# Kernel tuning notes

Measured on AMD Instinct MI355X. Metric: run time of the kernel, lower is better.

The kernel has to match this reference:

```python
import jax, jax.numpy as jnp
import numpy as np

B, D, N_CLASSES = 8192, 128, 512
MARGIN, GAMMA = 0.25, 256.0
NEG_INF = -1e9  # effectively -inf; logits are O(gamma*2) ~ 512 in magnitude


def setup_inputs() -> dict:
    key = jax.random.key(0)
    k1, k2 = jax.random.split(key)
    feat = jax.random.normal(k1, (B, D), dtype=jnp.float32)
    label = jax.random.randint(k2, (B,), 0, N_CLASSES, dtype=jnp.int64)
    return {"feat": feat, "label": label}


def reference(feat, label):
    m, gamma = MARGIN, GAMMA
    O_p, O_n = 1.0 + m, -m
    delta_p, delta_n = 1.0 - m, m

    # L2-normalize rows (eps clamp as in F.normalize)
    norm = jnp.maximum(jnp.linalg.norm(feat, axis=1, keepdims=True), 1e-12)
    f = feat / norm
    sim = f @ f.T  # [B, B]

    same = label[:, None] == label[None, :]
    eye = jnp.eye(sim.shape[0], dtype=bool)
    pos_mask = same & ~eye
    neg_mask = ~same

    sim_d = jax.lax.stop_gradient(sim)  # .detach() in torch
    alpha_p = jax.nn.relu(O_p - sim_d)
    alpha_n = jax.nn.relu(sim_d - O_n)

    logit_p = -gamma * alpha_p * (sim - delta_p)
    logit_n = gamma * alpha_n * (sim - delta_n)

    # Per-row masked logsumexp over positives / negatives
    lse_p = jax.nn.logsumexp(jnp.where(pos_mask, logit_p, NEG_INF), axis=1)
    lse_n = jax.nn.logsumexp(jnp.where(neg_mask, logit_n, NEG_INF), axis=1)

    # Rows with no positives or no negatives are skipped in the original loop
    valid = pos_mask.any(axis=1) & neg_mask.any(axis=1)
    loss_i = jax.nn.softplus(lse_n + lse_p)
    n_valid = jnp.maximum(valid.sum(), 1)
    return jnp.sum(jnp.where(valid, loss_i, 0.0)) / n_valid
```

## Files before the change

### kernel.cpp

```cpp
#include <hip/hip_runtime.h>
#include <hip/hip_bf16.h>

typedef short bf16x8 __attribute__((ext_vector_type(8)));
typedef float f32x4 __attribute__((ext_vector_type(4)));

#define B_ROWS 8192
#define DIM 128
#define NCLS 512
#define MMAX 64
#define NSLICE 32
#define NEG_BLOCKS 1024

#define G2 369.32993f
#define LN2F 0.69314718056f

__global__ __launch_bounds__(256) void prep_k(const float* __restrict__ feat,
                                              const int* __restrict__ label,
                                              unsigned short* __restrict__ fb,
                                              float* __restrict__ fnorm,
                                              int* __restrict__ cls_cnt,
                                              int* __restrict__ member) {
    const int wv = threadIdx.x >> 6, ln = threadIdx.x & 63;
    const int row = blockIdx.x * 4 + wv;
    const float2* fr = (const float2*)(feat + row * DIM);
    float2 v = fr[ln];
    float ss = v.x * v.x + v.y * v.y;
    #pragma unroll
    for (int d = 1; d < 64; d <<= 1) ss += __shfl_xor(ss, d);
    const float inv = 1.0f / fmaxf(sqrtf(ss), 1e-12f);
    const float x = v.x * inv, y = v.y * inv;
    ((float2*)fnorm)[row * 64 + ln] = make_float2(x, y);
    __hip_bfloat16 hx = __float2bfloat16(x), hy = __float2bfloat16(y);
    unsigned int ux = *(unsigned short*)&hx, uy = *(unsigned short*)&hy;
    ((unsigned int*)fb)[row * 64 + ln] = ux | (uy << 16);

    if (blockIdx.x < 32) {
        const int idx = blockIdx.x * 256 + threadIdx.x;
        const int lbl = label[idx];
        const int p = atomicAdd(&cls_cnt[lbl], 1);
        if (p < MMAX) member[lbl * MMAX + p] = idx;
    }
}

__device__ __forceinline__ void epi4(f32x4 acc, float& M, float& S,
                                     bool diag, int lc, int lg) {
    float u0 = acc[0] + 0.25f; float w0 = fmaf(G2, acc[0], -0.25f * G2);
    float u1 = acc[1] + 0.25f; float w1 = fmaf(G2, acc[1], -0.25f * G2);
    float u2 = acc[2] + 0.25f; float w2 = fmaf(G2, acc[2], -0.25f * G2);
    float u3 = acc[3] + 0.25f; float w3 = fmaf(G2, acc[3], -0.25f * G2);
    float l0 = fmaxf(u0, 0.f) * w0, l1 = fmaxf(u1, 0.f) * w1;
    float l2 = fmaxf(u2, 0.f) * w2, l3 = fmaxf(u3, 0.f) * w3;
    if (diag) {
        const int base = lg * 4;
        l0 = (base + 0 == lc) ? -3.0e8f : l0;
        l1 = (base + 1 == lc) ? -3.0e8f : l1;
        l2 = (base + 2 == lc) ? -3.0e8f : l2;
        l3 = (base + 3 == lc) ? -3.0e8f : l3;
    }
    const float gm = fmaxf(fmaxf(l0, l1), fmaxf(l2, l3));
    if (__any(gm > M - 25.f)) {
        const float Mn = fmaxf(M, gm);
        const float r  = __builtin_amdgcn_exp2f(M - Mn);
        const float e0 = __builtin_amdgcn_exp2f(l0 - Mn);
        const float e1 = __builtin_amdgcn_exp2f(l1 - Mn);
        const float e2 = __builtin_amdgcn_exp2f(l2 - Mn);
        const float e3 = __builtin_amdgcn_exp2f(l3 - Mn);
        S = fmaf(S, r, e0) + e1 + e2 + e3;
        M = Mn;
    }
}

__global__ __launch_bounds__(256) void main_k(const unsigned short* __restrict__ fb,
                                              const float* __restrict__ fnorm,
                                              const int* __restrict__ cls_cnt,
                                              const int* __restrict__ member,
                                              float* __restrict__ partials,
                                              float* __restrict__ lse2_p,
                                              float* __restrict__ lse2_same) {
    __shared__ float F[MMAX][DIM + 1];
    __shared__ int rl[MMAX];
    const int bid = blockIdx.x;

    if (bid < NEG_BLOCKS) {
        const int slice = bid & 31;
        const int mblk  = bid >> 5;
        const int wv = threadIdx.x >> 6, ln = threadIdx.x & 63;
        const int lc = ln & 15, lg = ln >> 4;
        const int mb = mblk * 256 + wv * 64;
        const bf16x8* fv = (const bf16x8*)fb;

        bf16x8 a[4][4];
        #pragma unroll
        for (int mi = 0; mi < 4; ++mi)
            #pragma unroll
            for (int k = 0; k < 4; ++k)
                a[mi][k] = fv[(mb + mi * 16 + lc) * 16 + lg + 4 * k];

        float M[4], S[4];
        #pragma unroll
        for (int mi = 0; mi < 4; ++mi) { M[mi] = -1e30f; S[mi] = 0.f; }

        const int nbase = slice * 256;
        bf16x8 bA[4], bB[4];

        #define LOADB(dst, n0) { \
            _Pragma("unroll") \
            for (int k = 0; k < 4; ++k) dst[k] = fv[((n0) + lc) * 16 + lg + 4 * k]; }

        #define STEP(bR, n0) { \
            f32x4 acc[4]; \
            _Pragma("unroll") \
            for (int mi = 0; mi < 4; ++mi) acc[mi] = (f32x4){0.f, 0.f, 0.f, 0.f}; \
            _Pragma("unroll") \
            for (int k = 0; k < 4; ++k) { \
                _Pragma("unroll") \
                for (int mi = 0; mi < 4; ++mi) \
                    acc[mi] = __builtin_amdgcn_mfma_f32_16x16x32_bf16(bR[k], a[mi][k], acc[mi], 0, 0, 0); \
            } \
            _Pragma("unroll") \
            for (int mi = 0; mi < 4; ++mi) \
                epi4(acc[mi], M[mi], S[mi], (n0) == mb + mi * 16, lc, lg); }

        LOADB(bA, nbase);
        #pragma unroll 1
        for (int t = 0; t < 16; t += 2) {
            LOADB(bB, nbase + (t + 1) * 16);
            STEP(bA, nbase + t * 16);
            if (t + 2 < 16) LOADB(bA, nbase + (t + 2) * 16);
            STEP(bB, nbase + (t + 1) * 16);
        }
        #undef LOADB
        #undef STEP

        #pragma unroll
        for (int mi = 0; mi < 4; ++mi) {
            float Mm = M[mi], Ss = S[mi];
            #pragma unroll
            for (int d = 16; d < 64; d <<= 1) {
                float Mo = __shfl_xor(Mm, d), So = __shfl_xor(Ss, d);
                float Mn = fmaxf(Mm, Mo);
                Ss = Ss * __builtin_amdgcn_exp2f(Mm - Mn) + So * __builtin_amdgcn_exp2f(Mo - Mn);
                Mm = Mn;
            }
            if (lg == 0)
                partials[slice * B_ROWS + mb + mi * 16 + lc] = Mm + __builtin_amdgcn_logf(Ss);
        }
    } else {
        const int c = bid - NEG_BLOCKS;
        const int tid = threadIdx.x;
        const int total = cls_cnt[c];
        const int m = total < MMAX ? total : MMAX;
        if (m == 0) return;
        const bool row_valid = (total >= 2);

        for (int r = tid; r < m; r += 256) rl[r] = member[c * MMAX + r];
        __syncthreads();
        for (int idx = tid; idx < m * DIM; idx += 256) {
            const int r = idx >> 7, d = idx & 127;
            F[r][d] = fnorm[rl[r] * DIM + d];
        }
        __syncthreads();

        const int wv = tid >> 6, ln = tid & 63;
        for (int i = wv; i < m; i += 4) {
            float s = 0.f;
            if (ln < m) {
                #pragma unroll 8
                for (int k = 0; k < DIM; ++k) s = fmaf(F[i][k], F[ln][k], s);
            }
            const bool act = (ln < m) && (ln != i);
            float up = 1.25f - s; float lp = act ? G2 * fmaxf(up, 0.f) * (up - 0.5f) : -1e30f;
            float un = s + 0.25f; float lnn = act ? G2 * fmaxf(un, 0.f) * (un - 0.5f) : -1e30f;
            float Mp = lp, Mn = lnn;
            #pragma unroll
            for (int d = 1; d < 64; d <<= 1) {
                Mp = fmaxf(Mp, __shfl_xor(Mp, d));
                Mn = fmaxf(Mn, __shfl_xor(Mn, d));
            }
            float Sp = act ? __builtin_amdgcn_exp2f(lp - Mp) : 0.f;
            float Sn = act ? __builtin_amdgcn_exp2f(lnn - Mn) : 0.f;
            #pragma unroll
            for (int d = 1; d < 64; d <<= 1) { Sp += __shfl_xor(Sp, d); Sn += __shfl_xor(Sn, d); }
            if (ln == 0) {
                const int row = rl[i];
                lse2_p[row]    = row_valid ? (Mp + __builtin_amdgcn_logf(Sp)) : -1e30f;
                lse2_same[row] = row_valid ? (Mn + __builtin_amdgcn_logf(Sn)) : -1e30f;
            }
        }
    }
}

__global__ __launch_bounds__(256) void finalize_k(const float* __restrict__ partials,
                                                  const float* __restrict__ lse2_p,
                                                  const float* __restrict__ lse2_same,
                                                  float* __restrict__ gsum,
                                                  int* __restrict__ gcnt,
                                                  int* __restrict__ done,
                                                  float* __restrict__ out) {
    const int r = blockIdx.x * 256 + threadIdx.x;
    float local = 0.f; int c = 0;
    const float lp2 = lse2_p[r];
    if (lp2 > -1e29f) {
        float p[NSLICE], mx = -1e30f;
        #pragma unroll
        for (int s = 0; s < NSLICE; ++s) { p[s] = partials[s * B_ROWS + r]; mx = fmaxf(mx, p[s]); }
        float Sa = 0.f;
        #pragma unroll
        for (int s = 0; s < NSLICE; ++s) Sa += __builtin_amdgcn_exp2f(p[s] - mx);
        const float lse2_all = mx + __builtin_amdgcn_logf(Sa);
        const float d = lse2_same[r] - lse2_all;
        const float corr = __builtin_amdgcn_logf(fmaxf(1.f - __builtin_amdgcn_exp2f(d), 1e-30f));
        const float z = LN2F * (lp2 + lse2_all + corr);
        local = fmaxf(z, 0.f) + log1pf(expf(-fabsf(z)));
        c = 1;
    }
    #pragma unroll
    for (int d = 1; d < 64; d <<= 1) { local += __shfl_xor(local, d); c += __shfl_xor(c, d); }
    __shared__ float wsum[4];
    __shared__ int wcnt[4];
    const int wv = threadIdx.x >> 6;
    if ((threadIdx.x & 63) == 0) { wsum[wv] = local; wcnt[wv] = c; }
    __syncthreads();
    if (threadIdx.x == 0) {
        const float ts = wsum[0] + wsum[1] + wsum[2] + wsum[3];
        const int tc = wcnt[0] + wcnt[1] + wcnt[2] + wcnt[3];
        atomicAdd(gsum, ts);
        atomicAdd(gcnt, tc);
        __threadfence();
        const int ticket = atomicAdd(done, 1);
        if (ticket == (int)gridDim.x - 1) {
            const float gs = atomicAdd(gsum, 0.0f);
            const int gc = atomicAdd(gcnt, 0);
            out[0] = gs / (float)(gc > 1 ? gc : 1);
        }
    }
}

extern "C" void kernel_launch(void* const* d_in, const int* in_sizes, int n_in,
                              void* d_out, int out_size, void* d_ws, size_t ws_size,
                              hipStream_t stream) {
    const float* feat = (const float*)d_in[0];
    const int* label = (const int*)d_in[1];
    float* out = (float*)d_out;
    char* ws = (char*)d_ws;

    unsigned short* fb = (unsigned short*)(ws);
    float* fnorm      = (float*)(ws + (2u << 20));
    float* partials   = (float*)(ws + (6u << 20));
    char*  tail       = ws + (7u << 20);
    float* lse2_p     = (float*)(tail);
    float* lse2_same  = (float*)(tail + 32768);
    int*   member     = (int*)  (tail + 65536);
    int*   cls_cnt    = (int*)  (tail + 196608);
    float* gsum       = (float*)(tail + 198656);
    int*   gcnt       = (int*)  (tail + 198660);
    int*   done       = (int*)  (tail + 198664);

    hipMemsetAsync(cls_cnt, 0, 2048 + 12, stream);

    prep_k<<<B_ROWS / 4, 256, 0, stream>>>(feat, label, fb, fnorm, cls_cnt, member);
    main_k<<<NEG_BLOCKS + NCLS, 256, 0, stream>>>(fb, fnorm, cls_cnt, member,
                                                  partials, lse2_p, lse2_same);
    finalize_k<<<B_ROWS / 256, 256, 0, stream>>>(partials, lse2_p, lse2_same,
                                                 gsum, gcnt, done, out);
}
```

Baseline: 122.6 us.

## Fuse finalize into neg kernel, move positive-class work into prep, pack fragments

```diff
diff --git a/kernel.cpp b/kernel.cpp
--- a/kernel.cpp
+++ b/kernel.cpp
@@ -10,35 +10,105 @@
 #define MMAX 64
 #define NSLICE 32
 #define NEG_BLOCKS 1024
+#define FIN_BLOCKS 32
 
 #define G2 369.32993f
 #define LN2F 0.69314718056f
 
 __global__ __launch_bounds__(256) void prep_k(const float* __restrict__ feat,
                                               const int* __restrict__ label,
-                                              unsigned short* __restrict__ fb,
-                                              float* __restrict__ fnorm,
-                                              int* __restrict__ cls_cnt,
-                                              int* __restrict__ member) {
-    const int wv = threadIdx.x >> 6, ln = threadIdx.x & 63;
-    const int row = blockIdx.x * 4 + wv;
-    const float2* fr = (const float2*)(feat + row * DIM);
-    float2 v = fr[ln];
-    float ss = v.x * v.x + v.y * v.y;
-    #pragma unroll
-    for (int d = 1; d < 64; d <<= 1) ss += __shfl_xor(ss, d);
-    const float inv = 1.0f / fmaxf(sqrtf(ss), 1e-12f);
-    const float x = v.x * inv, y = v.y * inv;
-    ((float2*)fnorm)[row * 64 + ln] = make_float2(x, y);
-    __hip_bfloat16 hx = __float2bfloat16(x), hy = __float2bfloat16(y);
-    unsigned int ux = *(unsigned short*)&hx, uy = *(unsigned short*)&hy;
-    ((unsigned int*)fb)[row * 64 + ln] = ux | (uy << 16);
-
-    if (blockIdx.x < 32) {
-        const int idx = blockIdx.x * 256 + threadIdx.x;
-        const int lbl = label[idx];
-        const int p = atomicAdd(&cls_cnt[lbl], 1);
-        if (p < MMAX) member[lbl * MMAX + p] = idx;
+                                              unsigned int* __restrict__ fbp,
+                                              float* __restrict__ lse2_p,
+                                              float* __restrict__ lse2_same,
+                                              int* __restrict__ ctrl) {
+    const int bid = blockIdx.x;
+    const int tid = threadIdx.x;
+    const int wv = tid >> 6, ln = tid & 63;
+
+    if (bid < 2048) {
+        if (bid == 0 && tid < 4) ctrl[tid] = 0;
+        const int row = bid * 4 + wv;
+        const float2 v = ((const float2*)feat)[row * 64 + ln];
+        float ss = v.x * v.x + v.y * v.y;
+        #pragma unroll
+        for (int d = 1; d < 64; d <<= 1) ss += __shfl_xor(ss, d);
+        const float inv = 1.0f / fmaxf(sqrtf(ss), 1e-12f);
+        const float x = v.x * inv, y = v.y * inv;
+        __hip_bfloat16 hx = __float2bfloat16(x), hy = __float2bfloat16(y);
+        const unsigned int ux = *(const unsigned short*)&hx;
+        const unsigned int uy = *(const unsigned short*)&hy;
+        const int T = row >> 4, lc = row & 15, c = ln >> 2, j = ln & 3;
+        const int frag16 = (T * 4 + (c >> 2)) * 64 + (c & 3) * 16 + lc;
+        fbp[frag16 * 4 + j] = ux | (uy << 16);
+        return;
+    }
+
+    const int c = bid - 2048;
+    __shared__ int rl[MMAX];
+    __shared__ int s_total;
+    __shared__ float F[MMAX][DIM + 1];
+
+    if (wv == 0) {
+        int base = 0;
+        for (int it = 0; it < 32; ++it) {
+            const int4 L = ((const int4*)label)[it * 64 + ln];
+            const int lv[4] = {L.x, L.y, L.z, L.w};
+            #pragma unroll
+            for (int j = 0; j < 4; ++j) {
+                const bool hit = (lv[j] == c);
+                const unsigned long long mask = __ballot(hit);
+                const int below = __popcll(mask & ((1ull << ln) - 1ull));
+                const int slot = base + below;
+                if (hit && slot < MMAX) rl[slot] = (it * 64 + ln) * 4 + j;
+                base += __popcll(mask);
+            }
+        }
+        if (ln == 0) s_total = base;
+    }
+    __syncthreads();
+    const int total = s_total;
+    const int m = total < MMAX ? total : MMAX;
+    if (m == 0) return;
+    const bool row_valid = (total >= 2);
+
+    for (int i = wv; i < m; i += 4) {
+        const int r = rl[i];
+        const float2 v = ((const float2*)feat)[r * 64 + ln];
+        float ss = v.x * v.x + v.y * v.y;
+        #pragma unroll
+        for (int d = 1; d < 64; d <<= 1) ss += __shfl_xor(ss, d);
+        const float inv = 1.0f / fmaxf(sqrtf(ss), 1e-12f);
+        F[i][2 * ln] = v.x * inv;
+        F[i][2 * ln + 1] = v.y * inv;
+    }
+    __syncthreads();
+
+    for (int i = wv; i < m; i += 4) {
+        float s = 0.f;
+        if (ln < m) {
+            #pragma unroll 8
+            for (int k = 0; k < DIM; ++k) s = fmaf(F[i][k], F[ln][k], s);
+        }
+        const bool act = (ln < m) && (ln != i);
+        const float up = 1.25f - s;
+        const float lp = act ? G2 * fmaxf(up, 0.f) * (up - 0.5f) : -1e30f;
+        const float un = s + 0.25f;
+        const float lnn = act ? G2 * fmaxf(un, 0.f) * (un - 0.5f) : -1e30f;
+        float Mp = lp, Mn = lnn;
+        #pragma unroll
+        for (int d = 1; d < 64; d <<= 1) {
+            Mp = fmaxf(Mp, __shfl_xor(Mp, d));
+            Mn = fmaxf(Mn, __shfl_xor(Mn, d));
+        }
+        float Sp = act ? __builtin_amdgcn_exp2f(lp - Mp) : 0.f;
+        float Sn = act ? __builtin_amdgcn_exp2f(lnn - Mn) : 0.f;
+        #pragma unroll
+        for (int d = 1; d < 64; d <<= 1) { Sp += __shfl_xor(Sp, d); Sn += __shfl_xor(Sn, d); }
+        if (ln == 0) {
+            const int row = rl[i];
+            lse2_p[row]    = row_valid ? (Mp + __builtin_amdgcn_logf(Sp)) : -1e30f;
+            lse2_same[row] = row_valid ? (Mn + __builtin_amdgcn_logf(Sn)) : -1e30f;
+        }
     }
 }
 
@@ -70,140 +140,105 @@
     }
 }
 
-__global__ __launch_bounds__(256) void main_k(const unsigned short* __restrict__ fb,
-                                              const float* __restrict__ fnorm,
-                                              const int* __restrict__ cls_cnt,
-                                              const int* __restrict__ member,
-                                              float* __restrict__ partials,
-                                              float* __restrict__ lse2_p,
-                                              float* __restrict__ lse2_same) {
-    __shared__ float F[MMAX][DIM + 1];
-    __shared__ int rl[MMAX];
+__global__ __launch_bounds__(256, 4) void neg_k(const unsigned short* __restrict__ fb_,
+                                                const float* __restrict__ lse2_p,
+                                                const float* __restrict__ lse2_same,
+                                                float* __restrict__ partials,
+                                                int* __restrict__ ctrl,
+                                                float* __restrict__ out) {
     const int bid = blockIdx.x;
-
-    if (bid < NEG_BLOCKS) {
-        const int slice = bid & 31;
-        const int mblk  = bid >> 5;
-        const int wv = threadIdx.x >> 6, ln = threadIdx.x & 63;
-        const int lc = ln & 15, lg = ln >> 4;
-        const int mb = mblk * 256 + wv * 64;
-        const bf16x8* fv = (const bf16x8*)fb;
-
-        bf16x8 a[4][4];
-        #pragma unroll
-        for (int mi = 0; mi < 4; ++mi)
-            #pragma unroll
-            for (int k = 0; k < 4; ++k)
-                a[mi][k] = fv[(mb + mi * 16 + lc) * 16 + lg + 4 * k];
-
-        float M[4], S[4];
-        #pragma unroll
-        for (int mi = 0; mi < 4; ++mi) { M[mi] = -1e30f; S[mi] = 0.f; }
-
-        const int nbase = slice * 256;
-        bf16x8 bA[4], bB[4];
-
-        #define LOADB(dst, n0) { \
-            _Pragma("unroll") \
-            for (int k = 0; k < 4; ++k) dst[k] = fv[((n0) + lc) * 16 + lg + 4 * k]; }
-
-        #define STEP(bR, n0) { \
-            f32x4 acc[4]; \
-            _Pragma("unroll") \
-            for (int mi = 0; mi < 4; ++mi) acc[mi] = (f32x4){0.f, 0.f, 0.f, 0.f}; \
-            _Pragma("unroll") \
-            for (int k = 0; k < 4; ++k) { \
-                _Pragma("unroll") \
-                for (int mi = 0; mi < 4; ++mi) \
-                    acc[mi] = __builtin_amdgcn_mfma_f32_16x16x32_bf16(bR[k], a[mi][k], acc[mi], 0, 0, 0); \
-            } \
+    const int tid = threadIdx.x;
+    const int wv = tid >> 6, ln = tid & 63;
+    const int lc = ln & 15, lg = ln >> 4;
+    const int slice = bid & 31, mblk = bid >> 5;
+    const int mb = mblk * 256 + wv * 64;
+    const int mbT = mb >> 4;
+    const bf16x8* pk = (const bf16x8*)fb_;
+    __shared__ int s_ticket;
+    __shared__ float wsum[4];
+    __shared__ int wcnt[4];
+
+    bf16x8 a[4][4];
+    #pragma unroll
+    for (int mi = 0; mi < 4; ++mi)
+        #pragma unroll
+        for (int k = 0; k < 4; ++k)
+            a[mi][k] = pk[((mbT + mi) * 4 + k) * 64 + ln];
+
+    float M[4], S[4];
+    #pragma unroll
+    for (int mi = 0; mi < 4; ++mi) { M[mi] = -1e30f; S[mi] = 0.f; }
+
+    const int nT0 = slice * 16;
+    bf16x8 bA[4], bB[4];
+
+    #define LOADB(dst, nT) { \
+        _Pragma("unroll") \
+        for (int k = 0; k < 4; ++k) dst[k] = pk[((nT) * 4 + k) * 64 + ln]; }
+
+    #define STEP(bR, nT) { \
+        f32x4 acc[4]; \
+        _Pragma("unroll") \
+        for (int mi = 0; mi < 4; ++mi) acc[mi] = (f32x4){0.f, 0.f, 0.f, 0.f}; \
+        _Pragma("unroll") \
+        for (int k = 0; k < 4; ++k) { \
             _Pragma("unroll") \
             for (int mi = 0; mi < 4; ++mi) \
-                epi4(acc[mi], M[mi], S[mi], (n0) == mb + mi * 16, lc, lg); }
-
-        LOADB(bA, nbase);
-        #pragma unroll 1
-        for (int t = 0; t < 16; t += 2) {
-            LOADB(bB, nbase + (t + 1) * 16);
-            STEP(bA, nbase + t * 16);
-            if (t + 2 < 16) LOADB(bA, nbase + (t + 2) * 16);
-            STEP(bB, nbase + (t + 1) * 16);
-        }
-        #undef LOADB
-        #undef STEP
-
-        #pragma unroll
-        for (int mi = 0; mi < 4; ++mi) {
-            float Mm = M[mi], Ss = S[mi];
-            #pragma unroll
-            for (int d = 16; d < 64; d <<= 1) {
-                float Mo = __shfl_xor(Mm, d), So = __shfl_xor(Ss, d);
-                float Mn = fmaxf(Mm, Mo);
-                Ss = Ss * __builtin_amdgcn_exp2f(Mm - Mn) + So * __builtin_amdgcn_exp2f(Mo - Mn);
-                Mm = Mn;
-            }
-            if (lg == 0)
-                partials[slice * B_ROWS + mb + mi * 16 + lc] = Mm + __builtin_amdgcn_logf(Ss);
-        }
-    } else {
-        const int c = bid - NEG_BLOCKS;
-        const int tid = threadIdx.x;
-        const int total = cls_cnt[c];
-        const int m = total < MMAX ? total : MMAX;
-        if (m == 0) return;
-        const bool row_valid = (total >= 2);
-
-        for (int r = tid; r < m; r += 256) rl[r] = member[c * MMAX + r];
-        __syncthreads();
-        for (int idx = tid; idx < m * DIM; idx += 256) {
-            const int r = idx >> 7, d = idx & 127;
-            F[r][d] = fnorm[rl[r] * DIM + d];
-        }
-        __syncthreads();
-
-        const int wv = tid >> 6, ln = tid & 63;
-        for (int i = wv; i < m; i += 4) {
-            float s = 0.f;
-            if (ln < m) {
-                #pragma unroll 8
-                for (int k = 0; k < DIM; ++k) s = fmaf(F[i][k], F[ln][k], s);
-            }
-            const bool act = (ln < m) && (ln != i);
-            float up = 1.25f - s; float lp = act ? G2 * fmaxf(up, 0.f) * (up - 0.5f) : -1e30f;
-            float un = s + 0.25f; float lnn = act ? G2 * fmaxf(un, 0.f) * (un - 0.5f) : -1e30f;
-            float Mp = lp, Mn = lnn;
-            #pragma unroll
-            for (int d = 1; d < 64; d <<= 1) {
-                Mp = fmaxf(Mp, __shfl_xor(Mp, d));
-                Mn = fmaxf(Mn, __shfl_xor(Mn, d));
-            }
-            float Sp = act ? __builtin_amdgcn_exp2f(lp - Mp) : 0.f;
-            float Sn = act ? __builtin_amdgcn_exp2f(lnn - Mn) : 0.f;
-            #pragma unroll
-            for (int d = 1; d < 64; d <<= 1) { Sp += __shfl_xor(Sp, d); Sn += __shfl_xor(Sn, d); }
-            if (ln == 0) {
-                const int row = rl[i];
-                lse2_p[row]    = row_valid ? (Mp + __builtin_amdgcn_logf(Sp)) : -1e30f;
-                lse2_same[row] = row_valid ? (Mn + __builtin_amdgcn_logf(Sn)) : -1e30f;
-            }
-        }
-    }
-}
-
-__global__ __launch_bounds__(256) void finalize_k(const float* __restrict__ partials,
-                                                  const float* __restrict__ lse2_p,
-                                                  const float* __restrict__ lse2_same,
-                                                  float* __restrict__ gsum,
-                                                  int* __restrict__ gcnt,
-                                                  int* __restrict__ done,
-                                                  float* __restrict__ out) {
-    const int r = blockIdx.x * 256 + threadIdx.x;
-    float local = 0.f; int c = 0;
+                acc[mi] = __builtin_amdgcn_mfma_f32_16x16x32_bf16(bR[k], a[mi][k], acc[mi], 0, 0, 0); \
+        } \
+        _Pragma("unroll") \
+        for (int mi = 0; mi < 4; ++mi) \
+            epi4(acc[mi], M[mi], S[mi], (nT) * 16 == mb + mi * 16, lc, lg); }
+
+    LOADB(bA, nT0);
+    #pragma unroll 1
+    for (int t = 0; t < 16; t += 2) {
+        LOADB(bB, nT0 + t + 1);
+        STEP(bA, nT0 + t);
+        if (t + 2 < 16) LOADB(bA, nT0 + t + 2);
+        STEP(bB, nT0 + t + 1);
+    }
+    #undef LOADB
+    #undef STEP
+
+    #pragma unroll
+    for (int mi = 0; mi < 4; ++mi) {
+        float Mm = M[mi], Ss = S[mi];
+        #pragma unroll
+        for (int d = 16; d < 64; d <<= 1) {
+            const float Mo = __shfl_xor(Mm, d), So = __shfl_xor(Ss, d);
+            const float Mn = fmaxf(Mm, Mo);
+            Ss = Ss * __builtin_amdgcn_exp2f(Mm - Mn) + So * __builtin_amdgcn_exp2f(Mo - Mn);
+            Mm = Mn;
+        }
+        if (lg == 0)
+            partials[slice * B_ROWS + mb + mi * 16 + lc] = Mm + __builtin_amdgcn_logf(Ss);
+    }
+
+    __threadfence();
+    if (tid == 0) s_ticket = atomicAdd(&ctrl[0], 1);
+    __syncthreads();
+    const int ticket = s_ticket;
+    if (ticket < NEG_BLOCKS - FIN_BLOCKS) return;
+
+    if (tid == 0) {
+        while (__hip_atomic_load(&ctrl[0], __ATOMIC_ACQUIRE, __HIP_MEMORY_SCOPE_AGENT)
+               < NEG_BLOCKS)
+            __builtin_amdgcn_s_sleep(8);
+    }
+    __syncthreads();
+
+    const int r = (ticket - (NEG_BLOCKS - FIN_BLOCKS)) * 256 + tid;
+    float local = 0.f; int cnt = 0;
     const float lp2 = lse2_p[r];
     if (lp2 > -1e29f) {
         float p[NSLICE], mx = -1e30f;
         #pragma unroll
-        for (int s = 0; s < NSLICE; ++s) { p[s] = partials[s * B_ROWS + r]; mx = fmaxf(mx, p[s]); }
+        for (int s = 0; s < NSLICE; ++s) {
+            p[s] = __hip_atomic_load(&partials[s * B_ROWS + r],
+                                     __ATOMIC_RELAXED, __HIP_MEMORY_SCOPE_AGENT);
+            mx = fmaxf(mx, p[s]);
+        }
         float Sa = 0.f;
         #pragma unroll
         for (int s = 0; s < NSLICE; ++s) Sa += __builtin_amdgcn_exp2f(p[s] - mx);
@@ -212,25 +247,23 @@
         const float corr = __builtin_amdgcn_logf(fmaxf(1.f - __builtin_amdgcn_exp2f(d), 1e-30f));
         const float z = LN2F * (lp2 + lse2_all + corr);
         local = fmaxf(z, 0.f) + log1pf(expf(-fabsf(z)));
-        c = 1;
-    }
-    #pragma unroll
-    for (int d = 1; d < 64; d <<= 1) { local += __shfl_xor(local, d); c += __shfl_xor(c, d); }
-    __shared__ float wsum[4];
-    __shared__ int wcnt[4];
-    const int wv = threadIdx.x >> 6;
-    if ((threadIdx.x & 63) == 0) { wsum[wv] = local; wcnt[wv] = c; }
-    __syncthreads();
-    if (threadIdx.x == 0) {
+        cnt = 1;
+    }
+    #pragma unroll
+    for (int d = 1; d < 64; d <<= 1) { local += __shfl_xor(local, d); cnt += __shfl_xor(cnt, d); }
+    if (ln == 0) { wsum[wv] = local; wcnt[wv] = cnt; }
+    __syncthreads();
+    if (tid == 0) {
         const float ts = wsum[0] + wsum[1] + wsum[2] + wsum[3];
         const int tc = wcnt[0] + wcnt[1] + wcnt[2] + wcnt[3];
-        atomicAdd(gsum, ts);
-        atomicAdd(gcnt, tc);
+        atomicAdd((float*)&ctrl[2], ts);
+        atomicAdd(&ctrl[3], tc);
         __threadfence();
-        const int ticket = atomicAdd(done, 1);
-        if (ticket == (int)gridDim.x - 1) {
-            const float gs = atomicAdd(gsum, 0.0f);
-            const int gc = atomicAdd(gcnt, 0);
+        const int t2 = atomicAdd(&ctrl[1], 1);
+        if (t2 == FIN_BLOCKS - 1) {
+            __threadfence();
+            const float gs = atomicAdd((float*)&ctrl[2], 0.0f);
+            const int gc = atomicAdd(&ctrl[3], 0);
             out[0] = gs / (float)(gc > 1 ? gc : 1);
         }
     }
@@ -244,23 +277,13 @@
     float* out = (float*)d_out;
     char* ws = (char*)d_ws;
 
-    unsigned short* fb = (unsigned short*)(ws);
-    float* fnorm      = (float*)(ws + (2u << 20));
-    float* partials   = (float*)(ws + (6u << 20));
-    char*  tail       = ws + (7u << 20);
-    float* lse2_p     = (float*)(tail);
-    float* lse2_same  = (float*)(tail + 32768);
-    int*   member     = (int*)  (tail + 65536);
-    int*   cls_cnt    = (int*)  (tail + 196608);
-    float* gsum       = (float*)(tail + 198656);
-    int*   gcnt       = (int*)  (tail + 198660);
-    int*   done       = (int*)  (tail + 198664);
-
-    hipMemsetAsync(cls_cnt, 0, 2048 + 12, stream);
-
-    prep_k<<<B_ROWS / 4, 256, 0, stream>>>(feat, label, fb, fnorm, cls_cnt, member);
-    main_k<<<NEG_BLOCKS + NCLS, 256, 0, stream>>>(fb, fnorm, cls_cnt, member,
-                                                  partials, lse2_p, lse2_same);
-    finalize_k<<<B_ROWS / 256, 256, 0, stream>>>(partials, lse2_p, lse2_same,
-                                                 gsum, gcnt, done, out);
-}
+    unsigned int* fbp = (unsigned int*)(ws);
+    float* partials   = (float*)(ws + (2u << 20));
+    float* lse2_p     = (float*)(ws + (3u << 20));
+    float* lse2_same  = (float*)(ws + (3u << 20) + 32768);
+    int*   ctrl       = (int*)  (ws + (3u << 20) + 65536);
+
+    prep_k<<<2048 + NCLS, 256, 0, stream>>>(feat, label, fbp, lse2_p, lse2_same, ctrl);
+    neg_k<<<NEG_BLOCKS, 256, 0, stream>>>((const unsigned short*)fbp, lse2_p, lse2_same,
+                                          partials, ctrl, out);
+}
```

Measured after the change: 203.5 us. 1.66x slower.
